# Kernel optimization log

Measured on AMD Instinct MI355X. Metric: run time of the kernel, lower is better.

The kernel has to match this reference:

```python
import jax, jax.numpy as jnp
import numpy as np
from jax import lax

STRIDE = 4
SCALES = (32.0, 64.0, 128.0)
RATIOS = (0.5, 1.0, 2.0)
PRE_NMS = 6000          # pre_nms_top_n['testing']
POST_NMS = 1000         # post_nms_top_n['testing']
NMS_THRESH = 0.7
MIN_SIZE = 1.0


def make_anchors(fh, fw):
    # 9 base anchors per cell (3 scales x 3 ratios), xyxy centered at cell centers.
    base = []
    for s in SCALES:
        for r in RATIOS:
            w = s * np.sqrt(1.0 / r)
            h = s * np.sqrt(r)
            base.append([-w / 2, -h / 2, w / 2, h / 2])
    base = np.asarray(base, np.float32)                      # [9,4]
    xs = (np.arange(fw, dtype=np.float32) + 0.5) * STRIDE
    ys = (np.arange(fh, dtype=np.float32) + 0.5) * STRIDE
    cx, cy = np.meshgrid(xs, ys)                             # [fh,fw]
    shifts = np.stack([cx, cy, cx, cy], -1)[:, :, None, :]   # [fh,fw,1,4]
    return jnp.asarray((shifts + base[None, None]).reshape(-1, 4))  # [fh*fw*9,4]


def conv(x, w, b):
    y = lax.conv_general_dilated(x, w, (1, 1), 'SAME',
                                 dimension_numbers=('NCHW', 'OIHW', 'NCHW'))
    return y + b[None, :, None, None]


def decode(anchors, deltas):
    wa = anchors[:, 2] - anchors[:, 0]
    ha = anchors[:, 3] - anchors[:, 1]
    cxa = anchors[:, 0] + 0.5 * wa
    cya = anchors[:, 1] + 0.5 * ha
    cx = deltas[:, 0] * wa + cxa
    cy = deltas[:, 1] * ha + cya
    w = jnp.exp(deltas[:, 2]) * wa
    h = jnp.exp(deltas[:, 3]) * ha
    return jnp.stack([cx - 0.5 * w, cy - 0.5 * h, cx + 0.5 * w, cy + 0.5 * h], -1)


def pairwise_iou(a, b):
    area_a = (a[:, 2] - a[:, 0]) * (a[:, 3] - a[:, 1])
    area_b = (b[:, 2] - b[:, 0]) * (b[:, 3] - b[:, 1])
    lt = jnp.maximum(a[:, None, :2], b[None, :, :2])
    rb = jnp.minimum(a[:, None, 2:], b[None, :, 2:])
    wh = jnp.clip(rb - lt, 0.0)
    inter = wh[..., 0] * wh[..., 1]
    return inter / (area_a[:, None] + area_b[None, :] - inter + 1e-9)


def nms_keep(boxes, valid, thresh):
    # boxes already sorted by score descending; greedy suppression.
    n = boxes.shape[0]
    iou = pairwise_iou(boxes, boxes)  # [n,n]
    def body(i, keep):
        suppressed = jnp.any((iou[i] > thresh) & keep)
        return keep.at[i].set(valid[i] & ~suppressed)
    return lax.fori_loop(0, n, body, jnp.zeros(n, bool))


def rpn_forward(feature, w1, b1, w_cls, b_cls, w_reg, b_reg, image_h, image_w,
                detach_for_proposal=True):
    fh, fw = feature.shape[2], feature.shape[3]
    x = jax.nn.relu(conv(feature, w1, b1))
    conf = conv(x, w_cls, b_cls).transpose(0, 2, 3, 1).reshape(-1)        # [N]
    offsets = conv(x, w_reg, b_reg).transpose(0, 2, 3, 1).reshape(-1, 4)  # [N,4]
    if detach_for_proposal:  # original detaches before create_proposal
        conf = lax.stop_gradient(conf)
        offsets = lax.stop_gradient(offsets)
    anchors = make_anchors(fh, fw)

    pre_n = min(PRE_NMS, conf.shape[0])
    scores, idx = lax.top_k(conf, pre_n)
    props = decode(anchors[idx], offsets[idx])
    # process_box: clip to image, drop boxes smaller than min_size (mask form)
    props = jnp.stack([jnp.clip(props[:, 0], 0.0, float(image_w)),
                       jnp.clip(props[:, 1], 0.0, float(image_h)),
                       jnp.clip(props[:, 2], 0.0, float(image_w)),
                       jnp.clip(props[:, 3], 0.0, float(image_h))], -1)
    valid = ((props[:, 2] - props[:, 0]) >= MIN_SIZE) & \
            ((props[:, 3] - props[:, 1]) >= MIN_SIZE)

    keep = nms_keep(lax.stop_gradient(props), valid, NMS_THRESH)
    # compact first POST_NMS kept boxes into a fixed-shape output (zero padded)
    rank = jnp.cumsum(keep) - 1
    dest = jnp.where(keep & (rank < POST_NMS), rank, POST_NMS)
    out = jnp.zeros((POST_NMS + 1, 4), props.dtype).at[dest].set(props)[:POST_NMS]
    return out


def setup_inputs() -> dict:
    key = jax.random.key(0)
    ks = jax.random.split(key, 4)
    return {
        'feature': jax.random.normal(ks[0], (1, 256, 200, 272), jnp.float32),
        'w1': jax.random.normal(ks[1], (256, 256, 3, 3), jnp.float32) * 0.02,
        'b1': jnp.zeros((256,), jnp.float32),
        'w_cls': jax.random.normal(ks[2], (9, 256, 1, 1), jnp.float32) * 0.02,
        'b_cls': jnp.zeros((9,), jnp.float32),
        'w_reg': jax.random.normal(ks[3], (36, 256, 1, 1), jnp.float32) * 0.01,
        'b_reg': jnp.zeros((36,), jnp.float32),
        'image_h': 800,
        'image_w': 1088,
    }


def reference(feature, w1, b1, w_cls, b_cls, w_reg, b_reg, image_h, image_w):
    return rpn_forward(feature, w1, b1, w_cls, b_cls, w_reg, b_reg,
                       image_h, image_w, detach_for_proposal=True)
```

## Files before the change

kernel.cpp:

```cpp
#include <hip/hip_runtime.h>
#include <hip/hip_bf16.h>
#include <math.h>

#define H_ 200
#define W_ 272
#define C_ 256
#define HW 54400
#define NANCH 489600
#define PRE_N 6000
#define POST_N 1000
#define NWORDS 94
#define CHUNK_W 2720
#define SELCAP 16384
#define NSEG 8

#define X_OFF       0ull
#define CONF_OFF    55705600ull
#define HIST1_OFF   57664000ull
#define SEL_OFF     57926144ull
#define SCAL_OFF    58188288ull
#define TOPIDX_OFF  58254080ull
#define BOXES_OFF   58278080ull
#define VALID_OFF   58374080ull
#define MASK_OFF    58398080ull
#define HISTC_OFF   60757376ull
#define WCR_OFF     65269376ull
#define XT_OFF      65278592ull
#define WS_NEED_XT  (XT_OFF + 55705600ull)

__device__ __forceinline__ unsigned fkey(float fv) {
    unsigned u = __float_as_uint(fv);
    return (u & 0x80000000u) ? ~u : (u | 0x80000000u);
}

__global__ __launch_bounds__(256) void k_repack(const float* __restrict__ w1,
                                                float* __restrict__ w1r,
                                                unsigned* __restrict__ histc) {
    int d = blockIdx.x * 256 + threadIdx.x;
    if (d < NSEG * 65536) histc[d] = 0u;
    int o = d & 7;
    int q = d >> 3;
    int t = q % 9;
    int icg = q / 9;
    int wg8 = icg >> 8, ic = icg & 255;
    w1r[d] = w1[((size_t)(wg8 * 8 + o) * 256 + ic) * 9 + t];
}

__global__ __launch_bounds__(256) void k_conv1(const float* __restrict__ f,
                                               const float* __restrict__ w1r,
                                               const float* __restrict__ b1,
                                               float* __restrict__ xo,
                                               float* __restrict__ xt,
                                               unsigned* __restrict__ scal,
                                               unsigned long long* __restrict__ sel,
                                               const float* __restrict__ wcls,
                                               float* __restrict__ wcr) {
    __shared__ __align__(16) float sI[2][2880];
    int tid = threadIdx.x;
    int fb = blockIdx.x + 9 * (blockIdx.y + 25 * blockIdx.z);
    {
        int g = fb * 256 + tid;
        if (g < 64) scal[g] = 0u;
        else if (g < 32832) ((unsigned*)sel)[g - 64] = 0xFFFFFFFFu;
    }
    if (fb == 0) {
        for (int e = tid; e < 2304; e += 256) {
            int a = e / 256, c = e % 256;
            wcr[c * 9 + a] = wcls[e];
        }
    }
    int lane = tid & 63;
    int wgl = __builtin_amdgcn_readfirstlane(tid >> 6);
    int xg = lane & 7;
    int yg = lane >> 3;
    int X0 = blockIdx.x * 32;
    int Y0 = blockIdx.y * 8;
    int wg = blockIdx.z * 4 + wgl;
    int y = Y0 + yg;
    int xbase = X0 + xg * 4;

    int off[11]; int lds[11]; bool ok[11];
#pragma unroll
    for (int it = 0; it < 11; it++) {
        int l = tid + it * 256;
        int ci = l / 340; int r = l - ci * 340; int ry = r / 34; int rx = r - ry * 34;
        int gx = X0 - 1 + rx, gy = Y0 - 1 + ry;
        ok[it] = (l < CHUNK_W) && gx >= 0 && gx < W_ && gy >= 0 && gy < H_;
        off[it] = ci * HW + gy * W_ + gx;
        lds[it] = (ci * 10 + ry) * 36 + rx;
    }
    float rbuf[11];
#pragma unroll
    for (int it = 0; it < 11; it++)
        rbuf[it] = ok[it] ? f[off[it]] : 0.f;
#pragma unroll
    for (int it = 0; it < 11; it++)
        if (tid + it * 256 < CHUNK_W) sI[0][lds[it]] = rbuf[it];
    __syncthreads();

    float acc[8][4];
#pragma unroll
    for (int o = 0; o < 8; o++)
#pragma unroll
        for (int i = 0; i < 4; i++) acc[o][i] = 0.f;

    const float* wbase = w1r + (size_t)wg * (256 * 72);

    int cur = 0;
    for (int ic0 = 0; ic0 < 256; ic0 += 8) {
        if (ic0 < 248) {
            const float* fn = f + (size_t)(ic0 + 8) * HW;
#pragma unroll
            for (int it = 0; it < 11; it++)
                rbuf[it] = ok[it] ? fn[off[it]] : 0.f;
        }
        const float* sbuf = sI[cur];
        for (int ci = 0; ci < 8; ci++) {
            const float* wci = wbase + (ic0 + ci) * 72;
#pragma unroll
            for (int ky = 0; ky < 3; ky++) {
                const float* irow = &sbuf[(ci * 10 + yg + ky) * 36 + xg * 4];
                float4 va = *(const float4*)irow;
                float2 vb = *(const float2*)(irow + 4);
                float in[6] = {va.x, va.y, va.z, va.w, vb.x, vb.y};
#pragma unroll
                for (int kx = 0; kx < 3; kx++) {
                    const float* w8 = wci + (ky * 3 + kx) * 8;
#pragma unroll
                    for (int o = 0; o < 8; o++) {
                        float w = w8[o];
#pragma unroll
                        for (int i = 0; i < 4; i++)
                            acc[o][i] = fmaf(w, in[i + kx], acc[o][i]);
                    }
                }
            }
        }
        if (ic0 < 248) {
#pragma unroll
            for (int it = 0; it < 11; it++)
                if (tid + it * 256 < CHUNK_W) sI[cur ^ 1][lds[it]] = rbuf[it];
        }
        __syncthreads();
        cur ^= 1;
    }
    float vout[8][4];
#pragma unroll
    for (int o = 0; o < 8; o++) {
        float bv = b1[wg * 8 + o];
#pragma unroll
        for (int i = 0; i < 4; i++)
            vout[o][i] = fmaxf(acc[o][i] + bv, 0.f);
    }
#pragma unroll
    for (int o = 0; o < 8; o++) {
        int oc = wg * 8 + o;
        float* orow = xo + (size_t)oc * HW + y * W_ + xbase;
        if (xbase + 3 < W_) {
            *(float4*)orow = make_float4(vout[o][0], vout[o][1], vout[o][2], vout[o][3]);
        } else {
            for (int i = 0; i < 4; i++)
                if (xbase + i < W_) orow[i] = vout[o][i];
        }
    }
    if (xt) {
#pragma unroll
        for (int i = 0; i < 4; i++) {
            if (xbase + i < W_) {
                size_t px = (size_t)(y * W_ + xbase + i);
                *(float4*)&xt[px * 256 + wg * 8] =
                    make_float4(vout[0][i], vout[1][i], vout[2][i], vout[3][i]);
                *(float4*)&xt[px * 256 + wg * 8 + 4] =
                    make_float4(vout[4][i], vout[5][i], vout[6][i], vout[7][i]);
            }
        }
    }
}

__global__ __launch_bounds__(256) void k_cls(const float* __restrict__ x,
                                             const float* __restrict__ wcr,
                                             const float* __restrict__ bc,
                                             float* __restrict__ conf,
                                             unsigned* __restrict__ histc) {
    int p = blockIdx.x * 256 + threadIdx.x;
    if (p >= HW) return;
    unsigned* myh = histc + (blockIdx.x & (NSEG - 1)) * 65536;
    float acc[9];
#pragma unroll
    for (int a = 0; a < 9; a++) acc[a] = 0.f;
    for (int c0 = 0; c0 < 256; c0 += 8) {
        float xv8[8];
#pragma unroll
        for (int j = 0; j < 8; j++)
            xv8[j] = x[(c0 + j) * HW + p];
#pragma unroll
        for (int j = 0; j < 8; j++) {
            const float* wp = wcr + (c0 + j) * 9;
#pragma unroll
            for (int a = 0; a < 9; a++) acc[a] = fmaf(wp[a], xv8[j], acc[a]);
        }
    }
#pragma unroll
    for (int a = 0; a < 9; a++) {
        float v = acc[a] + bc[a];
        conf[p * 9 + a] = v;
        atomicAdd(&myh[fkey(v) >> 16], 1u);
    }
}

__global__ __launch_bounds__(1024) void k_scan(const unsigned* __restrict__ histc,
                                               unsigned* scal) {
    __shared__ unsigned ssum[1024];
    int t = threadIdx.x;
    int base = 65535 - t * 64;
    unsigned s = 0;
    for (int seg = 0; seg < NSEG; seg++) {
        const uint4* hp = (const uint4*)(histc + seg * 65536 + (base - 63));
#pragma unroll
        for (int k = 0; k < 16; k++) { uint4 v = hp[k]; s += v.x + v.y + v.z + v.w; }
    }
    ssum[t] = s;
    __syncthreads();
    for (int off = 1; off < 1024; off <<= 1) {
        unsigned v = (t >= off) ? ssum[t - off] : 0u;
        __syncthreads();
        ssum[t] += v;
        __syncthreads();
    }
    unsigned incl = ssum[t], excl = incl - s;
    if (excl < 6000u && 6000u <= incl) {
        unsigned run = excl;
        bool found = false;
        for (int pass = 0; pass < 2 && !found; pass++) {
            unsigned c32[32];
#pragma unroll
            for (int j = 0; j < 32; j++) {
                int idx = base - (pass * 32 + j);
                unsigned cj = 0;
#pragma unroll
                for (int seg = 0; seg < NSEG; seg++) cj += histc[seg * 65536 + idx];
                c32[j] = cj;
            }
            for (int j = 0; j < 32; j++) {
                if (run + c32[j] >= 6000u) {
                    scal[0] = (unsigned)(base - (pass * 32 + j));
                    scal[1] = run;
                    found = true;
                    break;
                }
                run += c32[j];
            }
        }
    }
}

__global__ __launch_bounds__(256) void k_gather(const float* __restrict__ conf,
                                                unsigned* scal, unsigned long long* sel) {
    __shared__ unsigned lcA, lcB, bA, bB;
    int n = blockIdx.x * 256 + threadIdx.x;
    bool inr = n < NANCH;
    if (threadIdx.x == 0) { lcA = 0u; lcB = 0u; }
    __syncthreads();
    unsigned B1 = scal[0], cnt1 = scal[1];
    unsigned key = 0, off = 0;
    int cls = 0;
    if (inr) {
        key = fkey(conf[n]);
        unsigned pre = key >> 16;
        if (pre > B1)       { cls = 1; off = atomicAdd(&lcA, 1u); }
        else if (pre == B1) { cls = 2; off = atomicAdd(&lcB, 1u); }
    }
    __syncthreads();
    if (threadIdx.x == 0) {
        bA = lcA ? atomicAdd(&scal[4], lcA) : 0u;
        bB = lcB ? atomicAdd(&scal[36], lcB) : 0u;
    }
    __syncthreads();
    if (cls) {
        unsigned long long kk = ((unsigned long long)(~key) << 32) | (unsigned)n;
        if (cls == 1) {
            sel[bA + off] = kk;
        } else {
            unsigned pos = cnt1 + bB + off;
            if (pos < SELCAP) sel[pos] = kk;
        }
    }
}

__global__ __launch_bounds__(256) void k_rank(const unsigned* __restrict__ scal,
                                              const unsigned long long* __restrict__ sel,
                                              unsigned* __restrict__ topidx) {
    __shared__ unsigned long long tile[2048];
    unsigned filled = scal[1] + scal[36];
    if (filled > SELCAP) filled = SELCAP;
    int i = blockIdx.x * 256 + threadIdx.x;
    unsigned long long mykey = sel[i];
    int rank = 0;
    for (int t0 = 0; t0 < SELCAP; t0 += 2048) {
        if (t0 >= (int)filled) break;
        __syncthreads();
        for (int l = threadIdx.x; l < 2048; l += 256)
            tile[l] = sel[t0 + l];
        __syncthreads();
        for (int l = 0; l < 2048; l += 4) {
            ulonglong2 p = *(const ulonglong2*)&tile[l];
            ulonglong2 q = *(const ulonglong2*)&tile[l + 2];
            rank += (p.x < mykey) + (p.y < mykey) + (q.x < mykey) + (q.y < mykey);
        }
    }
    if (i < (int)filled && rank < PRE_N)
        topidx[rank] = (unsigned)(mykey & 0xFFFFFFFFull);
}

__global__ __launch_bounds__(256) void k_prop(const float* __restrict__ x,
                                              const float* __restrict__ xt,
                                              const float* __restrict__ wreg,
                                              const float* __restrict__ breg,
                                              const unsigned* __restrict__ topidx,
                                              const int* __restrict__ imh, const int* __restrict__ imw,
                                              float* __restrict__ boxes, int* __restrict__ valid) {
    int r = blockIdx.x * 4 + (threadIdx.x >> 6);
    int lane = threadIdx.x & 63;
    unsigned n = topidx[r];
    int a = (int)(n % 9u); int p = (int)(n / 9u);
    const float* wr = wreg + (4 * a) * 256;
    float xv4[4], w0[4], w1[4], w2[4], w3[4];
    if (xt) {
        const float* xp = xt + (size_t)p * 256;
#pragma unroll
        for (int j = 0; j < 4; j++) {
            int c = lane + 64 * j;
            xv4[j] = xp[c];
            w0[j] = wr[c]; w1[j] = wr[256 + c]; w2[j] = wr[512 + c]; w3[j] = wr[768 + c];
        }
    } else {
#pragma unroll
        for (int j = 0; j < 4; j++) {
            int c = lane + 64 * j;
            xv4[j] = x[c * HW + p];
            w0[j] = wr[c]; w1[j] = wr[256 + c]; w2[j] = wr[512 + c]; w3[j] = wr[768 + c];
        }
    }
    float s0 = 0, s1 = 0, s2 = 0, s3 = 0;
#pragma unroll
    for (int j = 0; j < 4; j++) {
        s0 = fmaf(w0[j], xv4[j], s0);
        s1 = fmaf(w1[j], xv4[j], s1);
        s2 = fmaf(w2[j], xv4[j], s2);
        s3 = fmaf(w3[j], xv4[j], s3);
    }
#pragma unroll
    for (int off = 32; off >= 1; off >>= 1) {
        s0 += __shfl_down(s0, off);
        s1 += __shfl_down(s1, off);
        s2 += __shfl_down(s2, off);
        s3 += __shfl_down(s3, off);
    }
    if (lane == 0) {
        float dx = s0 + breg[4 * a], dy = s1 + breg[4 * a + 1];
        float dw = s2 + breg[4 * a + 2], dh = s3 + breg[4 * a + 3];
        int wi = p % W_, hi = p / W_;
        const double SC[3] = {32.0, 64.0, 128.0};
        const double RT[3] = {0.5, 1.0, 2.0};
        double sd = SC[a / 3], rd = RT[a % 3];
        double wb = sd * sqrt(1.0 / rd), hb = sd * sqrt(rd);
        float bx1 = (float)(-wb * 0.5), by1 = (float)(-hb * 0.5);
        float bx2 = (float)(wb * 0.5),  by2 = (float)(hb * 0.5);
        float cxs = ((float)wi + 0.5f) * 4.0f, cys = ((float)hi + 0.5f) * 4.0f;
        float x1a = cxs + bx1, y1a = cys + by1, x2a = cxs + bx2, y2a = cys + by2;
        float wa = x2a - x1a, ha = y2a - y1a;
        float cxa = x1a + 0.5f * wa, cya = y1a + 0.5f * ha;
        float cx = dx * wa + cxa, cy = dy * ha + cya;
        float ww = expf(dw) * wa, hh = expf(dh) * ha;
        float X1 = cx - 0.5f * ww, Y1 = cy - 0.5f * hh;
        float X2 = cx + 0.5f * ww, Y2 = cy + 0.5f * hh;
        float Wf = (float)(*imw), Hf = (float)(*imh);
        X1 = fminf(fmaxf(X1, 0.f), Wf); Y1 = fminf(fmaxf(Y1, 0.f), Hf);
        X2 = fminf(fmaxf(X2, 0.f), Wf); Y2 = fminf(fmaxf(Y2, 0.f), Hf);
        boxes[4 * r] = X1; boxes[4 * r + 1] = Y1; boxes[4 * r + 2] = X2; boxes[4 * r + 3] = Y2;
        valid[r] = ((X2 - X1) >= 1.0f && (Y2 - Y1) >= 1.0f) ? 1 : 0;
    }
}

__global__ __launch_bounds__(256) void k_mask(const float* __restrict__ boxes,
                                              unsigned long long* __restrict__ mask) {
    __shared__ float jb[256];
    int jw = blockIdx.x;
    if (jw * 64 + 63 < (int)blockIdx.y * 256) return;
    int i = blockIdx.y * 256 + threadIdx.x;
    {
        int idx = jw * 256 + threadIdx.x;
        jb[threadIdx.x] = (idx < PRE_N * 4) ? boxes[idx] : 0.f;
    }
    __syncthreads();
    if (i >= PRE_N) return;
    float4 ab = *(const float4*)&boxes[4 * i];
    float ax1 = ab.x, ay1 = ab.y, ax2 = ab.z, ay2 = ab.w;
    float aarea = (ax2 - ax1) * (ay2 - ay1);
    unsigned long long m = 0;
    int jbase = jw * 64;
    for (int b = 0; b < 64; b++) {
        int j = jbase + b;
        if (j <= i || j >= PRE_N) continue;
        float bx1 = jb[4 * b], by1 = jb[4 * b + 1], bx2 = jb[4 * b + 2], by2 = jb[4 * b + 3];
        float barea = (bx2 - bx1) * (by2 - by1);
        float xx1 = fmaxf(ax1, bx1), yy1 = fmaxf(ay1, by1);
        float xx2 = fminf(ax2, bx2), yy2 = fminf(ay2, by2);
        float w = fmaxf(xx2 - xx1, 0.f), h = fmaxf(yy2 - yy1, 0.f);
        float inter = w * h;
        float iou = inter / (aarea + barea - inter + 1e-9f);
        if (iou > 0.7f) m |= (1ull << b);
    }
    mask[(size_t)i * NWORDS + jw] = m;
}

__global__ __launch_bounds__(256) void k_scan_nms(const unsigned long long* __restrict__ mask,
                                                  const int* __restrict__ valid,
                                                  const float* __restrict__ boxes,
                                                  float* __restrict__ out) {
    __shared__ unsigned long long diag[NWORDS][64];
    __shared__ unsigned long long removed[NWORDS];
    __shared__ unsigned long long validw[NWORDS];
    __shared__ int keepList[POST_N];
    __shared__ int cnt;
    __shared__ unsigned long long keptbits;
    int t = threadIdx.x;
    if (t < NWORDS) { removed[t] = 0ull; validw[t] = 0ull; }
    if (t == 0) cnt = 0;
    __syncthreads();
    for (int l = t; l < NWORDS * 64; l += 256) {
        int w = l >> 6, b = l & 63;
        int i = w * 64 + b;
        diag[w][b] = (i < PRE_N) ? mask[(size_t)i * NWORDS + w] : 0ull;
    }
    for (int i = t; i < PRE_N; i += 256)
        if (valid[i]) atomicOr(&validw[i >> 6], 1ull << (i & 63));
    __syncthreads();
    for (int w = 0; w < NWORDS; w++) {
        unsigned long long candw = validw[w] & ~removed[w];
        if (!candw) continue;
        if (t < 64) {
            unsigned long long mydiag = diag[w][t];
            unsigned long long cand = candw;
            unsigned long long kb = 0ull;
            int c = cnt;
            while (cand && c < POST_N) {
                int b = __ffsll((unsigned long long)cand) - 1;
                unsigned long long sup = __shfl(mydiag, b);
                if (t == 0) keepList[c] = w * 64 + b;
                c++;
                kb |= 1ull << b;
                cand &= ~(1ull << b);
                cand &= ~sup;
            }
            if (t == 0) { cnt = c; keptbits = kb; }
        }
        __syncthreads();
        if (cnt >= POST_N) break;
        unsigned long long kb = keptbits;
        if (kb) {
            for (int w2 = w + 1 + t; w2 < NWORDS; w2 += 256) {
                unsigned long long acc2 = removed[w2];
                unsigned long long tt = kb;
                while (tt) {
                    int b = __ffsll((unsigned long long)tt) - 1;
                    tt &= tt - 1;
                    acc2 |= mask[(size_t)(w * 64 + b) * NWORDS + w2];
                }
                removed[w2] = acc2;
            }
        }
        __syncthreads();
    }
    __syncthreads();
    int c = cnt;
    for (int e = t; e < POST_N * 4; e += 256) {
        int r = e >> 2;
        out[e] = (r < c) ? boxes[4 * keepList[r] + (e & 3)] : 0.f;
    }
}

extern "C" void kernel_launch(void* const* d_in, const int* in_sizes, int n_in,
                              void* d_out, int out_size, void* d_ws, size_t ws_size,
                              hipStream_t stream) {
    const float* feature = (const float*)d_in[0];
    const float* w1   = (const float*)d_in[1];
    const float* b1   = (const float*)d_in[2];
    const float* wcls = (const float*)d_in[3];
    const float* bcls = (const float*)d_in[4];
    const float* wreg = (const float*)d_in[5];
    const float* breg = (const float*)d_in[6];
    const int* imh = (const int*)d_in[7];
    const int* imw = (const int*)d_in[8];

    char* ws = (char*)d_ws;
    float* xbuf  = (float*)(ws + X_OFF);
    float* conf  = (float*)(ws + CONF_OFF);
    unsigned* scal  = (unsigned*)(ws + SCAL_OFF);
    unsigned long long* sel = (unsigned long long*)(ws + SEL_OFF);
    unsigned* topidx = (unsigned*)(ws + TOPIDX_OFF);
    float* boxes = (float*)(ws + BOXES_OFF);
    int* valid   = (int*)(ws + VALID_OFF);
    unsigned long long* mask = (unsigned long long*)(ws + MASK_OFF);
    float* w1r = (float*)(ws + MASK_OFF);
    unsigned* histc = (unsigned*)(ws + HISTC_OFF);
    float* wcr = (float*)(ws + WCR_OFF);
    float* xt  = (ws_size >= WS_NEED_XT) ? (float*)(ws + XT_OFF) : (float*)0;
    float* outF = (float*)d_out;

    hipLaunchKernelGGL(k_repack, dim3(2304), dim3(256), 0, stream, w1, w1r, histc);
    hipLaunchKernelGGL(k_conv1,  dim3(9, 25, 8), dim3(256), 0, stream,
                       feature, w1r, b1, xbuf, xt, scal, sel, wcls, wcr);
    hipLaunchKernelGGL(k_cls,    dim3(213),  dim3(256), 0, stream, xbuf, wcr, bcls, conf, histc);
    hipLaunchKernelGGL(k_scan,   dim3(1),    dim3(1024), 0, stream, histc, scal);
    hipLaunchKernelGGL(k_gather, dim3(1913), dim3(256), 0, stream, conf, scal, sel);
    hipLaunchKernelGGL(k_rank,   dim3(64),   dim3(256), 0, stream, scal, sel, topidx);
    hipLaunchKernelGGL(k_prop,   dim3(1500), dim3(256), 0, stream, xbuf, xt, wreg, breg, topidx, imh, imw, boxes, valid);
    hipLaunchKernelGGL(k_mask,   dim3(NWORDS, 24), dim3(256), 0, stream, boxes, mask);
    hipLaunchKernelGGL(k_scan_nms, dim3(1), dim3(256), 0, stream, mask, valid, boxes, outF);
}
```

Baseline: 1.449 ms.

## Fuse cls head into conv1 via last-block-per-tile atomic counter

Removes the separate k_cls launch. A per-tile atomic counter lets the last of the 8 output-channel-group blocks for each spatial tile compute the 9 cls logits, write conf and update the histogram, while that tile's data is likely still in cache. The wcls repack moves into k_repack, which also zeroes the tile counters, and the histogram segment count doubles to cut atomic contention. This adds threadfences and a serialized tail in the last block of each tile, and the cls work now runs on only 225 blocks.

```diff
diff --git a/kernel.cpp b/kernel.cpp
--- a/kernel.cpp
+++ b/kernel.cpp
@@ -12,11 +12,11 @@
 #define NWORDS 94
 #define CHUNK_W 2720
 #define SELCAP 16384
-#define NSEG 8
+#define NSEG 16
 
 #define X_OFF       0ull
 #define CONF_OFF    55705600ull
-#define HIST1_OFF   57664000ull
+#define TILEC_OFF   57664000ull
 #define SEL_OFF     57926144ull
 #define SCAL_OFF    58188288ull
 #define TOPIDX_OFF  58254080ull
@@ -35,9 +35,17 @@
 
 __global__ __launch_bounds__(256) void k_repack(const float* __restrict__ w1,
                                                 float* __restrict__ w1r,
-                                                unsigned* __restrict__ histc) {
+                                                unsigned* __restrict__ histc,
+                                                unsigned* __restrict__ tilec,
+                                                const float* __restrict__ wcls,
+                                                float* __restrict__ wcr) {
     int d = blockIdx.x * 256 + threadIdx.x;
-    if (d < NSEG * 65536) histc[d] = 0u;
+    if (d < (NSEG * 65536) / 2) { uint2 z; z.x = 0u; z.y = 0u; ((uint2*)histc)[d] = z; }
+    if (d < 225) tilec[d] = 0u;
+    if (d < 2304) {
+        int a = d / 256, c = d % 256;
+        wcr[c * 9 + a] = wcls[d];
+    }
     int o = d & 7;
     int q = d >> 3;
     int t = q % 9;
@@ -53,21 +61,20 @@
                                                float* __restrict__ xt,
                                                unsigned* __restrict__ scal,
                                                unsigned long long* __restrict__ sel,
-                                               const float* __restrict__ wcls,
-                                               float* __restrict__ wcr) {
+                                               const float* __restrict__ wcr,
+                                               const float* __restrict__ bc,
+                                               float* __restrict__ conf,
+                                               unsigned* __restrict__ histc,
+                                               unsigned* __restrict__ tilec) {
     __shared__ __align__(16) float sI[2][2880];
+    __shared__ unsigned isLast;
     int tid = threadIdx.x;
     int fb = blockIdx.x + 9 * (blockIdx.y + 25 * blockIdx.z);
+    int tileId = blockIdx.x + 9 * blockIdx.y;
     {
         int g = fb * 256 + tid;
         if (g < 64) scal[g] = 0u;
         else if (g < 32832) ((unsigned*)sel)[g - 64] = 0xFFFFFFFFu;
-    }
-    if (fb == 0) {
-        for (int e = tid; e < 2304; e += 256) {
-            int a = e / 256, c = e % 256;
-            wcr[c * 9 + a] = wcls[e];
-        }
     }
     int lane = tid & 63;
     int wgl = __builtin_amdgcn_readfirstlane(tid >> 6);
@@ -175,34 +182,40 @@
             }
         }
     }
-}
-
-__global__ __launch_bounds__(256) void k_cls(const float* __restrict__ x,
-                                             const float* __restrict__ wcr,
-                                             const float* __restrict__ bc,
-                                             float* __restrict__ conf,
-                                             unsigned* __restrict__ histc) {
-    int p = blockIdx.x * 256 + threadIdx.x;
-    if (p >= HW) return;
-    unsigned* myh = histc + (blockIdx.x & (NSEG - 1)) * 65536;
-    float acc[9];
-#pragma unroll
-    for (int a = 0; a < 9; a++) acc[a] = 0.f;
+
+    __threadfence();
+    __syncthreads();
+    if (tid == 0) {
+        unsigned prev = atomicAdd(&tilec[tileId], 1u);
+        isLast = (prev == 7u) ? 1u : 0u;
+    }
+    __syncthreads();
+    if (!isLast) return;
+    __threadfence();
+
+    int pxc = X0 + (tid & 31);
+    int pyc = Y0 + (tid >> 5);
+    if (pxc >= W_) return;
+    int p = pyc * W_ + pxc;
+    unsigned* myh = histc + (fb & (NSEG - 1)) * 65536;
+    float acc9[9];
+#pragma unroll
+    for (int a = 0; a < 9; a++) acc9[a] = 0.f;
     for (int c0 = 0; c0 < 256; c0 += 8) {
         float xv8[8];
 #pragma unroll
         for (int j = 0; j < 8; j++)
-            xv8[j] = x[(c0 + j) * HW + p];
+            xv8[j] = xo[(c0 + j) * HW + p];
 #pragma unroll
         for (int j = 0; j < 8; j++) {
             const float* wp = wcr + (c0 + j) * 9;
 #pragma unroll
-            for (int a = 0; a < 9; a++) acc[a] = fmaf(wp[a], xv8[j], acc[a]);
+            for (int a = 0; a < 9; a++) acc9[a] = fmaf(wp[a], xv8[j], acc9[a]);
         }
     }
 #pragma unroll
     for (int a = 0; a < 9; a++) {
-        float v = acc[a] + bc[a];
+        float v = acc9[a] + bc[a];
         conf[p * 9 + a] = v;
         atomicAdd(&myh[fkey(v) >> 16], 1u);
     }
@@ -496,6 +509,7 @@
     char* ws = (char*)d_ws;
     float* xbuf  = (float*)(ws + X_OFF);
     float* conf  = (float*)(ws + CONF_OFF);
+    unsigned* tilec = (unsigned*)(ws + TILEC_OFF);
     unsigned* scal  = (unsigned*)(ws + SCAL_OFF);
     unsigned long long* sel = (unsigned long long*)(ws + SEL_OFF);
     unsigned* topidx = (unsigned*)(ws + TOPIDX_OFF);
@@ -508,10 +522,9 @@
     float* xt  = (ws_size >= WS_NEED_XT) ? (float*)(ws + XT_OFF) : (float*)0;
     float* outF = (float*)d_out;
 
-    hipLaunchKernelGGL(k_repack, dim3(2304), dim3(256), 0, stream, w1, w1r, histc);
+    hipLaunchKernelGGL(k_repack, dim3(2304), dim3(256), 0, stream, w1, w1r, histc, tilec, wcls, wcr);
     hipLaunchKernelGGL(k_conv1,  dim3(9, 25, 8), dim3(256), 0, stream,
-                       feature, w1r, b1, xbuf, xt, scal, sel, wcls, wcr);
-    hipLaunchKernelGGL(k_cls,    dim3(213),  dim3(256), 0, stream, xbuf, wcr, bcls, conf, histc);
+                       feature, w1r, b1, xbuf, xt, scal, sel, wcr, bcls, conf, histc, tilec);
     hipLaunchKernelGGL(k_scan,   dim3(1),    dim3(1024), 0, stream, histc, scal);
     hipLaunchKernelGGL(k_gather, dim3(1913), dim3(256), 0, stream, conf, scal, sel);
     hipLaunchKernelGGL(k_rank,   dim3(64),   dim3(256), 0, stream, scal, sel, topidx);
```

After: 1.703 ms. 17.5% more time.
